# Kernel optimization log

Measured on AMD Instinct MI355X. Metric: run time of the kernel, lower is better.

Reference implementation:

```python
import jax, jax.numpy as jnp
import numpy as np

N = 100000
IN_DIM = 128
HID = 128
HEADS = 2
OUT_DIM = 2
E = 800000
NEG_SLOPE = 0.2


def setup_inputs() -> dict:
    key = jax.random.key(0)
    ks = jax.random.split(key, 12)
    x = jax.random.normal(ks[0], (N, IN_DIM), dtype=jnp.float32)
    edge_index = jax.random.randint(ks[1], (2, E), 0, N, dtype=jnp.int64)
    s = 0.05
    # GATConv layer 1: in=128 -> heads=2, out=128
    W1 = jax.random.normal(ks[2], (IN_DIM, HEADS * HID), dtype=jnp.float32) * s
    a_src1 = jax.random.normal(ks[3], (HEADS, HID), dtype=jnp.float32) * s
    a_dst1 = jax.random.normal(ks[4], (HEADS, HID), dtype=jnp.float32) * s
    b1 = jnp.zeros((HEADS * HID,), dtype=jnp.float32)
    # GATConv layer 2: in=256 -> heads=2, out=128
    W2 = jax.random.normal(ks[5], (HEADS * HID, HEADS * HID), dtype=jnp.float32) * s
    a_src2 = jax.random.normal(ks[6], (HEADS, HID), dtype=jnp.float32) * s
    a_dst2 = jax.random.normal(ks[7], (HEADS, HID), dtype=jnp.float32) * s
    b2 = jnp.zeros((HEADS * HID,), dtype=jnp.float32)
    # post_mp: Linear(256,128) -> Dropout(eval, no-op) -> Linear(128,2)
    Wp1 = jax.random.normal(ks[8], (HEADS * HID, HID), dtype=jnp.float32) * s
    bp1 = jnp.zeros((HID,), dtype=jnp.float32)
    Wp2 = jax.random.normal(ks[9], (HID, OUT_DIM), dtype=jnp.float32) * s
    bp2 = jnp.zeros((OUT_DIM,), dtype=jnp.float32)
    return {"x": x, "edge_index": edge_index,
            "W1": W1, "a_src1": a_src1, "a_dst1": a_dst1, "b1": b1,
            "W2": W2, "a_src2": a_src2, "a_dst2": a_dst2, "b2": b2,
            "Wp1": Wp1, "bp1": bp1, "Wp2": Wp2, "bp2": bp2}


def gat_conv(x, src, dst, W, a_src, a_dst, b):
    # linear transform, split heads: [N, H, C]
    h = (x @ W).reshape(-1, HEADS, HID)
    # per-node attention logits: [N, H]
    alpha_src = jnp.sum(h * a_src, axis=-1)
    alpha_dst = jnp.sum(h * a_dst, axis=-1)
    # per-edge logits, edge e = (src -> dst): [E, H]
    e = jax.nn.leaky_relu(alpha_src[src] + alpha_dst[dst], NEG_SLOPE)
    # segment softmax over incoming edges of each destination node
    m = jax.ops.segment_max(e, dst, num_segments=N)
    e = jnp.exp(e - m[dst])
    denom = jax.ops.segment_sum(e, dst, num_segments=N)
    alpha = e / (denom[dst] + 1e-16)
    # gather source features, weight, scatter-add to destinations
    msg = h[src] * alpha[:, :, None]            # [E, H, C]
    out = jax.ops.segment_sum(msg, dst, num_segments=N)  # [N, H, C]
    return out.reshape(-1, HEADS * HID) + b


def reference(x, edge_index, W1, a_src1, a_dst1, b1, W2, a_src2, a_dst2, b2,
              Wp1, bp1, Wp2, bp2):
    # add self-loops (PyG GATConv default)
    loops = jnp.arange(N, dtype=edge_index.dtype)
    src = jnp.concatenate([edge_index[0], loops])
    dst = jnp.concatenate([edge_index[1], loops])
    h = jax.nn.relu(gat_conv(x, src, dst, W1, a_src1, a_dst1, b1))
    h = jax.nn.relu(gat_conv(h, src, dst, W2, a_src2, a_dst2, b2))
    h = h @ Wp1 + bp1          # post_mp Linear 1 (dropout is eval no-op)
    h = h @ Wp2 + bp2          # post_mp Linear 2
    return jax.nn.sigmoid(h)
```

## Files before the change

### kernel.cpp

```cpp
#include <hip/hip_runtime.h>
#include <hip/hip_bf16.h>
#include <math.h>

#define NNODES 100000
#define NPAD   100032
#define IN_DIM 128
#define HID 128
#define HEADS 2
#define F2 256
#define NEDGES 800000
#define ETOT 900000
#define NEG_SLOPE 0.2f

typedef unsigned int uint;
typedef unsigned short ushort;
typedef __attribute__((ext_vector_type(8))) short short8;
typedef __attribute__((ext_vector_type(4))) float floatx4;

__device__ __forceinline__ ushort f2bf(float f) {
    uint u = __builtin_bit_cast(uint, f);
    u += 0x7fffu + ((u >> 16) & 1u);
    return (ushort)(u >> 16);
}
__device__ __forceinline__ float bf2f(uint u16) {
    return __builtin_bit_cast(float, u16 << 16);
}
__device__ __forceinline__ float wred_sum(float v) {
    for (int o = 32; o; o >>= 1) v += __shfl_xor(v, o);
    return v;
}

__global__ __launch_bounds__(256) void hist_kernel(const int* __restrict__ ei,
                                                   int* __restrict__ deg) {
    int i = blockIdx.x * 256 + threadIdx.x;
    if (i >= ETOT) return;
    int dst = (i < NEDGES) ? ei[NEDGES + i] : (i - NEDGES);
    atomicAdd(&deg[dst], 1);
}

__global__ __launch_bounds__(256) void scan1_kernel(const int* __restrict__ deg,
                                                    int* __restrict__ row_start,
                                                    int* __restrict__ bsum) {
    __shared__ int s[256];
    int t = threadIdx.x;
    int i = blockIdx.x * 256 + t;
    int v = (i < NNODES) ? deg[i] : 0;
    s[t] = v;
    __syncthreads();
    for (int off = 1; off < 256; off <<= 1) {
        int x = (t >= off) ? s[t - off] : 0;
        __syncthreads();
        s[t] += x;
        __syncthreads();
    }
    if (i < NNODES) row_start[i] = s[t] - v;
    if (t == 255) bsum[blockIdx.x] = s[255];
}

__global__ __launch_bounds__(256) void scan_fix_kernel(int* __restrict__ row_start,
                                                       const int* __restrict__ bsum,
                                                       int* __restrict__ cursor) {
    __shared__ int sh[256];
    int t = threadIdx.x, bid = blockIdx.x;
    int v = 0;
    for (int k = t; k < bid; k += 256) v += bsum[k];
    sh[t] = v;
    __syncthreads();
    for (int off = 128; off; off >>= 1) {
        if (t < off) sh[t] += sh[t + off];
        __syncthreads();
    }
    int boff = sh[0];
    int i = bid * 256 + t;
    if (i == 0) row_start[NNODES] = ETOT;
    if (i < NNODES) {
        int r = row_start[i] + boff;
        row_start[i] = r;
        cursor[i] = r;
    }
}

__global__ __launch_bounds__(256) void scatter_kernel(const int* __restrict__ ei,
                                                      int* __restrict__ cursor,
                                                      int* __restrict__ csr_src) {
    int i = blockIdx.x * 256 + threadIdx.x;
    if (i >= ETOT) return;
    int src, dst;
    if (i < NEDGES) { src = ei[i]; dst = ei[NEDGES + i]; }
    else            { src = i - NEDGES; dst = src; }
    int pos = atomicAdd(&cursor[dst], 1);
    csr_src[pos] = src;
}

__global__ __launch_bounds__(256) void prep_kernel(const float* __restrict__ W1,
                                                   ushort* __restrict__ W1t,
                                                   const float* __restrict__ W2,
                                                   ushort* __restrict__ W2t,
                                                   const float* __restrict__ Wp1,
                                                   const float* __restrict__ bp1,
                                                   const float* __restrict__ Wp2,
                                                   const float* __restrict__ bp2,
                                                   float2* __restrict__ Wf,
                                                   float* __restrict__ bfv,
                                                   int* __restrict__ deg) {
    int b = blockIdx.x, t = threadIdx.x;
    if (b < 128) {
        int i = b * 256 + t;
        int n = i >> 7, k = i & 127;
        W1t[n * 128 + k] = f2bf(W1[k * 256 + n]);
    } else if (b < 384) {
        int i = (b - 128) * 256 + t;
        int n = i >> 8, k = i & 255;
        W2t[n * 256 + k] = f2bf(W2[k * 256 + n]);
    } else if (b == 384) {
        float s0 = 0.f, s1 = 0.f;
        for (int m = 0; m < 128; m++) {
            float w = Wp1[t * 128 + m];
            s0 += w * Wp2[2 * m];
            s1 += w * Wp2[2 * m + 1];
        }
        Wf[t] = make_float2(s0, s1);
        if (t < 2) {
            float bb = bp2[t];
            for (int m = 0; m < 128; m++) bb += bp1[m] * Wp2[2 * m + t];
            bfv[t] = bb;
        }
    } else {
        int i = (b - 385) * 256 + t;
        if (i < NNODES) deg[i] = 0;
    }
}

__global__ __launch_bounds__(256) void mfma_gemm_f32A(const float* __restrict__ A,
                                                      const ushort* __restrict__ Bt,
                                                      ushort* __restrict__ C,
                                                      float* __restrict__ as_f,
                                                      float* __restrict__ ad_f,
                                                      const float* __restrict__ aS,
                                                      const float* __restrict__ aD,
                                                      int K) {
    __shared__ ushort As[64][40];
    __shared__ ushort Bs[128][40];
    int t = threadIdx.x;
    int wave = t >> 6, lane = t & 63;
    int quad = lane >> 4, l16 = lane & 15;
    size_t rowBase = (size_t)blockIdx.x * 64;
    int colBase = blockIdx.y * 128;
    int head = blockIdx.y;

    floatx4 acc[8];
#pragma unroll
    for (int i = 0; i < 8; i++) acc[i] = (floatx4){0.f, 0.f, 0.f, 0.f};

    int ar = t >> 2, ac = (t & 3) * 8;
    int agr = (int)rowBase + ar;
    const float*  Ap  = A + (size_t)agr * K + ac;
    const ushort* Bp0 = Bt + (size_t)(colBase + ar) * K + ac;
    const ushort* Bp1 = Bp0 + (size_t)64 * K;
    bool aok = agr < NNODES;

    for (int k0 = 0; k0 < K; k0 += 32) {
        float4 f0 = make_float4(0.f, 0.f, 0.f, 0.f), f1 = f0;
        if (aok) {
            f0 = *reinterpret_cast<const float4*>(Ap + k0);
            f1 = *reinterpret_cast<const float4*>(Ap + k0 + 4);
        }
        uint4 b0 = *reinterpret_cast<const uint4*>(Bp0 + k0);
        uint4 b1 = *reinterpret_cast<const uint4*>(Bp1 + k0);
        uint4 av;
        av.x = (uint)f2bf(f0.x) | ((uint)f2bf(f0.y) << 16);
        av.y = (uint)f2bf(f0.z) | ((uint)f2bf(f0.w) << 16);
        av.z = (uint)f2bf(f1.x) | ((uint)f2bf(f1.y) << 16);
        av.w = (uint)f2bf(f1.z) | ((uint)f2bf(f1.w) << 16);
        *reinterpret_cast<uint4*>(&As[ar][ac])      = av;
        *reinterpret_cast<uint4*>(&Bs[ar][ac])      = b0;
        *reinterpret_cast<uint4*>(&Bs[64 + ar][ac]) = b1;
        __syncthreads();

        union { uint4 u; short8 s; } afr, bfr;
        afr.u = *reinterpret_cast<const uint4*>(&As[wave * 16 + l16][quad * 8]);
#pragma unroll
        for (int nt = 0; nt < 8; nt++) {
            bfr.u = *reinterpret_cast<const uint4*>(&Bs[nt * 16 + l16][quad * 8]);
            acc[nt] = __builtin_amdgcn_mfma_f32_16x16x32_bf16(afr.s, bfr.s, acc[nt], 0, 0, 0);
        }
        __syncthreads();
    }

    {
        float aSv[8], aDv[8];
#pragma unroll
        for (int nt = 0; nt < 8; nt++) {
            int c = colBase + nt * 16 + l16;
            aSv[nt] = aS[c];
            aDv[nt] = aD[c];
        }
#pragma unroll
        for (int r = 0; r < 4; r++) {
            float ps = 0.f, pd = 0.f;
#pragma unroll
            for (int nt = 0; nt < 8; nt++) {
                ps += acc[nt][r] * aSv[nt];
                pd += acc[nt][r] * aDv[nt];
            }
#pragma unroll
            for (int o = 1; o < 16; o <<= 1) {
                ps += __shfl_xor(ps, o);
                pd += __shfl_xor(pd, o);
            }
            if (l16 == 0) {
                size_t row = rowBase + wave * 16 + quad * 4 + r;
                as_f[2 * row + head] = ps;
                ad_f[2 * row + head] = pd;
            }
        }
    }

    ushort* lbuf = &Bs[0][0];
#pragma unroll
    for (int half = 0; half < 2; half++) {
        __syncthreads();
#pragma unroll
        for (int nt4 = 0; nt4 < 4; nt4++) {
            int nt = half * 4 + nt4;
            int col = nt4 * 16 + l16;
#pragma unroll
            for (int r = 0; r < 4; r++) {
                int row = wave * 16 + quad * 4 + r;
                lbuf[row * 72 + col] = f2bf(acc[nt][r]);
            }
        }
        __syncthreads();
        int row = t >> 2;
        int ch = t & 3;
        uint4 v0 = *reinterpret_cast<const uint4*>(&lbuf[row * 72 + ch * 8]);
        uint4 v1 = *reinterpret_cast<const uint4*>(&lbuf[row * 72 + 32 + ch * 8]);
        size_t g = (rowBase + row) * (size_t)F2 + colBase + half * 64;
        *reinterpret_cast<uint4*>(&C[g + ch * 8]) = v0;
        *reinterpret_cast<uint4*>(&C[g + 32 + ch * 8]) = v1;
    }
}

__global__ __launch_bounds__(256) void mfma_gemm_bf16A(const ushort* __restrict__ A,
                                                       const ushort* __restrict__ Bt,
                                                       ushort* __restrict__ C,
                                                       float* __restrict__ as_f,
                                                       float* __restrict__ ad_f,
                                                       const float* __restrict__ aS,
                                                       const float* __restrict__ aD,
                                                       int K) {
    __shared__ ushort As[64][40];
    __shared__ ushort Bs[128][40];
    int t = threadIdx.x;
    int wave = t >> 6, lane = t & 63;
    int quad = lane >> 4, l16 = lane & 15;
    size_t rowBase = (size_t)blockIdx.x * 64;
    int colBase = blockIdx.y * 128;
    int head = blockIdx.y;

    floatx4 acc[8];
#pragma unroll
    for (int i = 0; i < 8; i++) acc[i] = (floatx4){0.f, 0.f, 0.f, 0.f};

    int ar = t >> 2, ac = (t & 3) * 8;
    const ushort* Ap  = A + (rowBase + ar) * K + ac;
    const ushort* Bp0 = Bt + (size_t)(colBase + ar) * K + ac;
    const ushort* Bp1 = Bp0 + (size_t)64 * K;

    for (int k0 = 0; k0 < K; k0 += 32) {
        uint4 av = *reinterpret_cast<const uint4*>(Ap + k0);
        uint4 b0 = *reinterpret_cast<const uint4*>(Bp0 + k0);
        uint4 b1 = *reinterpret_cast<const uint4*>(Bp1 + k0);
        *reinterpret_cast<uint4*>(&As[ar][ac])      = av;
        *reinterpret_cast<uint4*>(&Bs[ar][ac])      = b0;
        *reinterpret_cast<uint4*>(&Bs[64 + ar][ac]) = b1;
        __syncthreads();

        union { uint4 u; short8 s; } afr, bfr;
        afr.u = *reinterpret_cast<const uint4*>(&As[wave * 16 + l16][quad * 8]);
#pragma unroll
        for (int nt = 0; nt < 8; nt++) {
            bfr.u = *reinterpret_cast<const uint4*>(&Bs[nt * 16 + l16][quad * 8]);
            acc[nt] = __builtin_amdgcn_mfma_f32_16x16x32_bf16(afr.s, bfr.s, acc[nt], 0, 0, 0);
        }
        __syncthreads();
    }

    {
        float aSv[8], aDv[8];
#pragma unroll
        for (int nt = 0; nt < 8; nt++) {
            int c = colBase + nt * 16 + l16;
            aSv[nt] = aS[c];
            aDv[nt] = aD[c];
        }
#pragma unroll
        for (int r = 0; r < 4; r++) {
            float ps = 0.f, pd = 0.f;
#pragma unroll
            for (int nt = 0; nt < 8; nt++) {
                ps += acc[nt][r] * aSv[nt];
                pd += acc[nt][r] * aDv[nt];
            }
#pragma unroll
            for (int o = 1; o < 16; o <<= 1) {
                ps += __shfl_xor(ps, o);
                pd += __shfl_xor(pd, o);
            }
            if (l16 == 0) {
                size_t row = rowBase + wave * 16 + quad * 4 + r;
                as_f[2 * row + head] = ps;
                ad_f[2 * row + head] = pd;
            }
        }
    }

    ushort* lbuf = &Bs[0][0];
#pragma unroll
    for (int half = 0; half < 2; half++) {
        __syncthreads();
#pragma unroll
        for (int nt4 = 0; nt4 < 4; nt4++) {
            int nt = half * 4 + nt4;
            int col = nt4 * 16 + l16;
#pragma unroll
            for (int r = 0; r < 4; r++) {
                int row = wave * 16 + quad * 4 + r;
                lbuf[row * 72 + col] = f2bf(acc[nt][r]);
            }
        }
        __syncthreads();
        int row = t >> 2;
        int ch = t & 3;
        uint4 v0 = *reinterpret_cast<const uint4*>(&lbuf[row * 72 + ch * 8]);
        uint4 v1 = *reinterpret_cast<const uint4*>(&lbuf[row * 72 + 32 + ch * 8]);
        size_t g = (rowBase + row) * (size_t)F2 + colBase + half * 64;
        *reinterpret_cast<uint4*>(&C[g + ch * 8]) = v0;
        *reinterpret_cast<uint4*>(&C[g + 32 + ch * 8]) = v1;
    }
}

__device__ __forceinline__ float edge_w(float2 q, float adsel, bool head1) {
    float l = (head1 ? q.y : q.x) + adsel;
    l = l > 0.f ? l : NEG_SLOPE * l;
    return __expf(l);
}

__global__ __launch_bounds__(256) void gather_kernel(const uint2* __restrict__ hb2,
                                                     const int* __restrict__ row_start,
                                                     const int* __restrict__ csr_src,
                                                     const float2* __restrict__ as_,
                                                     const float2* __restrict__ ad_,
                                                     const float4* __restrict__ bias4,
                                                     uint2* __restrict__ outb2,
                                                     const float4* __restrict__ WfA,
                                                     const float* __restrict__ bfv,
                                                     float2* __restrict__ outp,
                                                     int final_mode) {
    int wave = threadIdx.x >> 6, lane = threadIdx.x & 63;
    int n = blockIdx.x * 4 + wave;
    if (n >= NNODES) return;
    int beg = row_start[n], end = row_start[n + 1];
    float2 ad = ad_[n];
    bool head1 = lane >= 32;
    float adsel = head1 ? ad.y : ad.x;

    float a0 = 0.f, a1 = 0.f, a2 = 0.f, a3 = 0.f;
    float aden = 0.f;

    int j = beg;
    for (; j + 3 < end; j += 4) {
        int s0 = csr_src[j],     s1 = csr_src[j + 1];
        int s2 = csr_src[j + 2], s3 = csr_src[j + 3];
        float2 q0 = as_[s0], q1 = as_[s1], q2 = as_[s2], q3 = as_[s3];
        uint2 h0 = hb2[(size_t)s0 * 64 + lane];
        uint2 h1 = hb2[(size_t)s1 * 64 + lane];
        uint2 h2 = hb2[(size_t)s2 * 64 + lane];
        uint2 h3 = hb2[(size_t)s3 * 64 + lane];
        float w0 = edge_w(q0, adsel, head1), w1 = edge_w(q1, adsel, head1);
        float w2 = edge_w(q2, adsel, head1), w3 = edge_w(q3, adsel, head1);
        aden += (w0 + w1) + (w2 + w3);
        a0 += w0 * bf2f(h0.x & 0xffffu) + w1 * bf2f(h1.x & 0xffffu)
            + w2 * bf2f(h2.x & 0xffffu) + w3 * bf2f(h3.x & 0xffffu);
        a1 += w0 * bf2f(h0.x >> 16) + w1 * bf2f(h1.x >> 16)
            + w2 * bf2f(h2.x >> 16) + w3 * bf2f(h3.x >> 16);
        a2 += w0 * bf2f(h0.y & 0xffffu) + w1 * bf2f(h1.y & 0xffffu)
            + w2 * bf2f(h2.y & 0xffffu) + w3 * bf2f(h3.y & 0xffffu);
        a3 += w0 * bf2f(h0.y >> 16) + w1 * bf2f(h1.y >> 16)
            + w2 * bf2f(h2.y >> 16) + w3 * bf2f(h3.y >> 16);
    }
    for (; j < end; j++) {
        int s = csr_src[j];
        float2 q = as_[s];
        uint2 hv = hb2[(size_t)s * 64 + lane];
        float w = edge_w(q, adsel, head1);
        aden += w;
        a0 += w * bf2f(hv.x & 0xffffu);
        a1 += w * bf2f(hv.x >> 16);
        a2 += w * bf2f(hv.y & 0xffffu);
        a3 += w * bf2f(hv.y >> 16);
    }

    float inv = 1.f / (aden + 1e-16f);
    float4 b = bias4[lane];
    float o0 = fmaxf(a0 * inv + b.x, 0.f);
    float o1 = fmaxf(a1 * inv + b.y, 0.f);
    float o2 = fmaxf(a2 * inv + b.z, 0.f);
    float o3 = fmaxf(a3 * inv + b.w, 0.f);
    if (!final_mode) {
        uint2 pk;
        pk.x = (uint)f2bf(o0) | ((uint)f2bf(o1) << 16);
        pk.y = (uint)f2bf(o2) | ((uint)f2bf(o3) << 16);
        outb2[(size_t)n * 64 + lane] = pk;
    } else {
        float4 wa = WfA[2 * lane];
        float4 wb = WfA[2 * lane + 1];
        float p0 = o0 * wa.x + o1 * wa.z + o2 * wb.x + o3 * wb.z;
        float p1 = o0 * wa.y + o1 * wa.w + o2 * wb.y + o3 * wb.w;
        p0 = wred_sum(p0);
        p1 = wred_sum(p1);
        if (lane == 0) {
            float2 r;
            r.x = 1.f / (1.f + __expf(-(p0 + bfv[0])));
            r.y = 1.f / (1.f + __expf(-(p1 + bfv[1])));
            outp[n] = r;
        }
    }
}

extern "C" void kernel_launch(void* const* d_in, const int* in_sizes, int n_in,
                              void* d_out, int out_size, void* d_ws, size_t ws_size,
                              hipStream_t stream) {
    const float* x      = (const float*)d_in[0];
    const int*   ei     = (const int*)d_in[1];
    const float* W1     = (const float*)d_in[2];
    const float* a_src1 = (const float*)d_in[3];
    const float* a_dst1 = (const float*)d_in[4];
    const float* b1     = (const float*)d_in[5];
    const float* W2     = (const float*)d_in[6];
    const float* a_src2 = (const float*)d_in[7];
    const float* a_dst2 = (const float*)d_in[8];
    const float* b2     = (const float*)d_in[9];
    const float* Wp1    = (const float*)d_in[10];
    const float* bp1    = (const float*)d_in[11];
    const float* Wp2    = (const float*)d_in[12];
    const float* bp2    = (const float*)d_in[13];
    float* outp = (float*)d_out;

    char* w = (char*)d_ws;
    ushort* hbf  = (ushort*)w; w += (size_t)NPAD * 256 * sizeof(ushort);
    ushort* obf  = (ushort*)w; w += (size_t)NPAD * 256 * sizeof(ushort);
    ushort* W1t  = (ushort*)w; w += (size_t)256 * 128 * sizeof(ushort);
    ushort* W2t  = (ushort*)w; w += (size_t)256 * 256 * sizeof(ushort);
    float2* Wf   = (float2*)w; w += 256 * sizeof(float2);
    float*  bfv  = (float*)w;  w += 4 * sizeof(float);
    float2* as_  = (float2*)w; w += (size_t)NPAD * sizeof(float2);
    float2* ad_  = (float2*)w; w += (size_t)NPAD * sizeof(float2);
    int* deg       = (int*)w; w += (size_t)NNODES * sizeof(int);
    int* row_start = (int*)w; w += (size_t)(NNODES + 16) * sizeof(int);
    int* cursor    = (int*)w; w += (size_t)NNODES * sizeof(int);
    int* csr_src   = (int*)w; w += (size_t)ETOT * sizeof(int);
    int* bsum      = (int*)w; w += 512 * sizeof(int);

    const int SCAN_BLOCKS = (NNODES + 255) / 256;
    const int NODE_WAVES  = (NNODES + 3) / 4;
    const int MB = NPAD / 64;

    prep_kernel<<<776, 256, 0, stream>>>(W1, W1t, W2, W2t, Wp1, bp1, Wp2, bp2,
                                         Wf, bfv, deg);

    hist_kernel<<<(ETOT + 255) / 256, 256, 0, stream>>>(ei, deg);
    scan1_kernel<<<SCAN_BLOCKS, 256, 0, stream>>>(deg, row_start, bsum);
    scan_fix_kernel<<<SCAN_BLOCKS, 256, 0, stream>>>(row_start, bsum, cursor);
    scatter_kernel<<<(ETOT + 255) / 256, 256, 0, stream>>>(ei, cursor, csr_src);

    mfma_gemm_f32A<<<dim3(MB, 2), 256, 0, stream>>>(x, W1t, hbf, (float*)as_, (float*)ad_,
                                                    a_src1, a_dst1, 128);
    gather_kernel<<<NODE_WAVES, 256, 0, stream>>>((const uint2*)hbf, row_start, csr_src,
                                                  as_, ad_, (const float4*)b1, (uint2*)obf,
                                                  (const float4*)Wf, bfv, (float2*)outp, 0);

    mfma_gemm_bf16A<<<dim3(MB, 2), 256, 0, stream>>>(obf, W2t, hbf, (float*)as_, (float*)ad_,
                                                     a_src2, a_dst2, 256);
    gather_kernel<<<NODE_WAVES, 256, 0, stream>>>((const uint2*)hbf, row_start, csr_src,
                                                  as_, ad_, (const float4*)b2, (uint2*)obf,
                                                  (const float4*)Wf, bfv, (float2*)outp, 1);
}
```

Baseline: 439.9 us.

## Double GEMM row tile to 128 so each wave computes two 16-row groups

Both MFMA GEMM kernels now process 128 rows per block instead of 64, and each wave keeps two sets of accumulators so every B fragment loaded from shared memory feeds two MFMAs. This halves B-tile global loads and LDS B reads per output, and halves the block count. NPAD grows to a multiple of 128 and the epilogue store is remapped to 128 rows. The cost is more accumulator registers, which may lower occupancy, and fewer blocks to spread over the CUs.

```diff
diff --git a/kernel.cpp b/kernel.cpp
--- a/kernel.cpp
+++ b/kernel.cpp
@@ -3,7 +3,7 @@
 #include <math.h>
 
 #define NNODES 100000
-#define NPAD   100032
+#define NPAD   100096
 #define IN_DIM 128
 #define HID 128
 #define HEADS 2
@@ -139,50 +139,64 @@
                                                       const float* __restrict__ aS,
                                                       const float* __restrict__ aD,
                                                       int K) {
-    __shared__ ushort As[64][40];
-    __shared__ ushort Bs[128][40];
+    __shared__ ushort smem[10240];
     int t = threadIdx.x;
     int wave = t >> 6, lane = t & 63;
     int quad = lane >> 4, l16 = lane & 15;
-    size_t rowBase = (size_t)blockIdx.x * 64;
+    size_t rowBase = (size_t)blockIdx.x * 128;
     int colBase = blockIdx.y * 128;
     int head = blockIdx.y;
 
-    floatx4 acc[8];
-#pragma unroll
-    for (int i = 0; i < 8; i++) acc[i] = (floatx4){0.f, 0.f, 0.f, 0.f};
+    floatx4 acc[2][8];
+#pragma unroll
+    for (int rg = 0; rg < 2; rg++)
+#pragma unroll
+        for (int i = 0; i < 8; i++) acc[rg][i] = (floatx4){0.f, 0.f, 0.f, 0.f};
 
     int ar = t >> 2, ac = (t & 3) * 8;
-    int agr = (int)rowBase + ar;
-    const float*  Ap  = A + (size_t)agr * K + ac;
+    int agr0 = (int)rowBase + ar;
+    const float*  Ap0 = A + (size_t)agr0 * K + ac;
+    const float*  Ap1 = Ap0 + (size_t)64 * K;
     const ushort* Bp0 = Bt + (size_t)(colBase + ar) * K + ac;
     const ushort* Bp1 = Bp0 + (size_t)64 * K;
-    bool aok = agr < NNODES;
+    bool aok0 = agr0 < NNODES;
+    bool aok1 = agr0 + 64 < NNODES;
 
     for (int k0 = 0; k0 < K; k0 += 32) {
-        float4 f0 = make_float4(0.f, 0.f, 0.f, 0.f), f1 = f0;
-        if (aok) {
-            f0 = *reinterpret_cast<const float4*>(Ap + k0);
-            f1 = *reinterpret_cast<const float4*>(Ap + k0 + 4);
+        float4 f0 = make_float4(0.f, 0.f, 0.f, 0.f), f1 = f0, f2 = f0, f3 = f0;
+        if (aok0) {
+            f0 = *reinterpret_cast<const float4*>(Ap0 + k0);
+            f1 = *reinterpret_cast<const float4*>(Ap0 + k0 + 4);
+        }
+        if (aok1) {
+            f2 = *reinterpret_cast<const float4*>(Ap1 + k0);
+            f3 = *reinterpret_cast<const float4*>(Ap1 + k0 + 4);
         }
         uint4 b0 = *reinterpret_cast<const uint4*>(Bp0 + k0);
         uint4 b1 = *reinterpret_cast<const uint4*>(Bp1 + k0);
-        uint4 av;
-        av.x = (uint)f2bf(f0.x) | ((uint)f2bf(f0.y) << 16);
-        av.y = (uint)f2bf(f0.z) | ((uint)f2bf(f0.w) << 16);
-        av.z = (uint)f2bf(f1.x) | ((uint)f2bf(f1.y) << 16);
-        av.w = (uint)f2bf(f1.z) | ((uint)f2bf(f1.w) << 16);
-        *reinterpret_cast<uint4*>(&As[ar][ac])      = av;
-        *reinterpret_cast<uint4*>(&Bs[ar][ac])      = b0;
-        *reinterpret_cast<uint4*>(&Bs[64 + ar][ac]) = b1;
-        __syncthreads();
-
-        union { uint4 u; short8 s; } afr, bfr;
-        afr.u = *reinterpret_cast<const uint4*>(&As[wave * 16 + l16][quad * 8]);
+        uint4 a0, a1;
+        a0.x = (uint)f2bf(f0.x) | ((uint)f2bf(f0.y) << 16);
+        a0.y = (uint)f2bf(f0.z) | ((uint)f2bf(f0.w) << 16);
+        a0.z = (uint)f2bf(f1.x) | ((uint)f2bf(f1.y) << 16);
+        a0.w = (uint)f2bf(f1.z) | ((uint)f2bf(f1.w) << 16);
+        a1.x = (uint)f2bf(f2.x) | ((uint)f2bf(f2.y) << 16);
+        a1.y = (uint)f2bf(f2.z) | ((uint)f2bf(f2.w) << 16);
+        a1.z = (uint)f2bf(f3.x) | ((uint)f2bf(f3.y) << 16);
+        a1.w = (uint)f2bf(f3.z) | ((uint)f2bf(f3.w) << 16);
+        *reinterpret_cast<uint4*>(&smem[ar * 40 + ac])          = a0;
+        *reinterpret_cast<uint4*>(&smem[(ar + 64) * 40 + ac])   = a1;
+        *reinterpret_cast<uint4*>(&smem[5120 + ar * 40 + ac])        = b0;
+        *reinterpret_cast<uint4*>(&smem[5120 + (ar + 64) * 40 + ac]) = b1;
+        __syncthreads();
+
+        union { uint4 u; short8 s; } afr0, afr1, bfr;
+        afr0.u = *reinterpret_cast<const uint4*>(&smem[(wave * 32 + l16) * 40 + quad * 8]);
+        afr1.u = *reinterpret_cast<const uint4*>(&smem[(wave * 32 + 16 + l16) * 40 + quad * 8]);
 #pragma unroll
         for (int nt = 0; nt < 8; nt++) {
-            bfr.u = *reinterpret_cast<const uint4*>(&Bs[nt * 16 + l16][quad * 8]);
-            acc[nt] = __builtin_amdgcn_mfma_f32_16x16x32_bf16(afr.s, bfr.s, acc[nt], 0, 0, 0);
+            bfr.u = *reinterpret_cast<const uint4*>(&smem[5120 + (nt * 16 + l16) * 40 + quad * 8]);
+            acc[0][nt] = __builtin_amdgcn_mfma_f32_16x16x32_bf16(afr0.s, bfr.s, acc[0][nt], 0, 0, 0);
+            acc[1][nt] = __builtin_amdgcn_mfma_f32_16x16x32_bf16(afr1.s, bfr.s, acc[1][nt], 0, 0, 0);
         }
         __syncthreads();
     }
@@ -196,27 +210,29 @@
             aDv[nt] = aD[c];
         }
 #pragma unroll
-        for (int r = 0; r < 4; r++) {
-            float ps = 0.f, pd = 0.f;
-#pragma unroll
-            for (int nt = 0; nt < 8; nt++) {
-                ps += acc[nt][r] * aSv[nt];
-                pd += acc[nt][r] * aDv[nt];
+        for (int rg = 0; rg < 2; rg++) {
+#pragma unroll
+            for (int r = 0; r < 4; r++) {
+                float ps = 0.f, pd = 0.f;
+#pragma unroll
+                for (int nt = 0; nt < 8; nt++) {
+                    ps += acc[rg][nt][r] * aSv[nt];
+                    pd += acc[rg][nt][r] * aDv[nt];
+                }
+#pragma unroll
+                for (int o = 1; o < 16; o <<= 1) {
+                    ps += __shfl_xor(ps, o);
+                    pd += __shfl_xor(pd, o);
+                }
+                if (l16 == 0) {
+                    size_t row = rowBase + wave * 32 + rg * 16 + quad * 4 + r;
+                    as_f[2 * row + head] = ps;
+                    ad_f[2 * row + head] = pd;
+                }
             }
-#pragma unroll
-            for (int o = 1; o < 16; o <<= 1) {
-                ps += __shfl_xor(ps, o);
-                pd += __shfl_xor(pd, o);
-            }
-            if (l16 == 0) {
-                size_t row = rowBase + wave * 16 + quad * 4 + r;
-                as_f[2 * row + head] = ps;
-                ad_f[2 * row + head] = pd;
-            }
-        }
-    }
-
-    ushort* lbuf = &Bs[0][0];
+        }
+    }
+
 #pragma unroll
     for (int half = 0; half < 2; half++) {
         __syncthreads();
@@ -225,19 +241,21 @@
             int nt = half * 4 + nt4;
             int col = nt4 * 16 + l16;
 #pragma unroll
-            for (int r = 0; r < 4; r++) {
-                int row = wave * 16 + quad * 4 + r;
-                lbuf[row * 72 + col] = f2bf(acc[nt][r]);
+            for (int rg = 0; rg < 2; rg++) {
+#pragma unroll
+                for (int r = 0; r < 4; r++) {
+                    int row = wave * 32 + rg * 16 + quad * 4 + r;
+                    smem[row * 72 + col] = f2bf(acc[rg][nt][r]);
+                }
             }
         }
         __syncthreads();
-        int row = t >> 2;
-        int ch = t & 3;
-        uint4 v0 = *reinterpret_cast<const uint4*>(&lbuf[row * 72 + ch * 8]);
-        uint4 v1 = *reinterpret_cast<const uint4*>(&lbuf[row * 72 + 32 + ch * 8]);
-        size_t g = (rowBase + row) * (size_t)F2 + colBase + half * 64;
-        *reinterpret_cast<uint4*>(&C[g + ch * 8]) = v0;
-        *reinterpret_cast<uint4*>(&C[g + 32 + ch * 8]) = v1;
+        int row = t >> 1;
+        int ch = (t & 1) * 4;
+        const uint4* src = reinterpret_cast<const uint4*>(&smem[row * 72]);
+        uint4 v0 = src[ch], v1 = src[ch + 1], v2 = src[ch + 2], v3 = src[ch + 3];
+        uint4* dst = reinterpret_cast<uint4*>(&C[(rowBase + row) * (size_t)F2 + colBase + half * 64]);
+        dst[ch] = v0; dst[ch + 1] = v1; dst[ch + 2] = v2; dst[ch + 3] = v3;
     }
 }
 
@@ -249,39 +267,45 @@
                                                        const float* __restrict__ aS,
                                                        const float* __restrict__ aD,
                                                        int K) {
-    __shared__ ushort As[64][40];
-    __shared__ ushort Bs[128][40];
+    __shared__ ushort smem[10240];
     int t = threadIdx.x;
     int wave = t >> 6, lane = t & 63;
     int quad = lane >> 4, l16 = lane & 15;
-    size_t rowBase = (size_t)blockIdx.x * 64;
+    size_t rowBase = (size_t)blockIdx.x * 128;
     int colBase = blockIdx.y * 128;
     int head = blockIdx.y;
 
-    floatx4 acc[8];
-#pragma unroll
-    for (int i = 0; i < 8; i++) acc[i] = (floatx4){0.f, 0.f, 0.f, 0.f};
+    floatx4 acc[2][8];
+#pragma unroll
+    for (int rg = 0; rg < 2; rg++)
+#pragma unroll
+        for (int i = 0; i < 8; i++) acc[rg][i] = (floatx4){0.f, 0.f, 0.f, 0.f};
 
     int ar = t >> 2, ac = (t & 3) * 8;
-    const ushort* Ap  = A + (rowBase + ar) * K + ac;
+    const ushort* Ap0 = A + (rowBase + ar) * K + ac;
+    const ushort* Ap1 = Ap0 + (size_t)64 * K;
     const ushort* Bp0 = Bt + (size_t)(colBase + ar) * K + ac;
     const ushort* Bp1 = Bp0 + (size_t)64 * K;
 
     for (int k0 = 0; k0 < K; k0 += 32) {
-        uint4 av = *reinterpret_cast<const uint4*>(Ap + k0);
+        uint4 a0 = *reinterpret_cast<const uint4*>(Ap0 + k0);
+        uint4 a1 = *reinterpret_cast<const uint4*>(Ap1 + k0);
         uint4 b0 = *reinterpret_cast<const uint4*>(Bp0 + k0);
         uint4 b1 = *reinterpret_cast<const uint4*>(Bp1 + k0);
-        *reinterpret_cast<uint4*>(&As[ar][ac])      = av;
-        *reinterpret_cast<uint4*>(&Bs[ar][ac])      = b0;
-        *reinterpret_cast<uint4*>(&Bs[64 + ar][ac]) = b1;
-        __syncthreads();
-
-        union { uint4 u; short8 s; } afr, bfr;
-        afr.u = *reinterpret_cast<const uint4*>(&As[wave * 16 + l16][quad * 8]);
+        *reinterpret_cast<uint4*>(&smem[ar * 40 + ac])          = a0;
+        *reinterpret_cast<uint4*>(&smem[(ar + 64) * 40 + ac])   = a1;
+        *reinterpret_cast<uint4*>(&smem[5120 + ar * 40 + ac])        = b0;
+        *reinterpret_cast<uint4*>(&smem[5120 + (ar + 64) * 40 + ac]) = b1;
+        __syncthreads();
+
+        union { uint4 u; short8 s; } afr0, afr1, bfr;
+        afr0.u = *reinterpret_cast<const uint4*>(&smem[(wave * 32 + l16) * 40 + quad * 8]);
+        afr1.u = *reinterpret_cast<const uint4*>(&smem[(wave * 32 + 16 + l16) * 40 + quad * 8]);
 #pragma unroll
         for (int nt = 0; nt < 8; nt++) {
-            bfr.u = *reinterpret_cast<const uint4*>(&Bs[nt * 16 + l16][quad * 8]);
-            acc[nt] = __builtin_amdgcn_mfma_f32_16x16x32_bf16(afr.s, bfr.s, acc[nt], 0, 0, 0);
+            bfr.u = *reinterpret_cast<const uint4*>(&smem[5120 + (nt * 16 + l16) * 40 + quad * 8]);
+            acc[0][nt] = __builtin_amdgcn_mfma_f32_16x16x32_bf16(afr0.s, bfr.s, acc[0][nt], 0, 0, 0);
+            acc[1][nt] = __builtin_amdgcn_mfma_f32_16x16x32_bf16(afr1.s, bfr.s, acc[1][nt], 0, 0, 0);
         }
         __syncthreads();
     }
@@ -295,27 +319,29 @@
             aDv[nt] = aD[c];
         }
 #pragma unroll
-        for (int r = 0; r < 4; r++) {
-            float ps = 0.f, pd = 0.f;
-#pragma unroll
-            for (int nt = 0; nt < 8; nt++) {
-                ps += acc[nt][r] * aSv[nt];
-                pd += acc[nt][r] * aDv[nt];
+        for (int rg = 0; rg < 2; rg++) {
+#pragma unroll
+            for (int r = 0; r < 4; r++) {
+                float ps = 0.f, pd = 0.f;
+#pragma unroll
+                for (int nt = 0; nt < 8; nt++) {
+                    ps += acc[rg][nt][r] * aSv[nt];
+                    pd += acc[rg][nt][r] * aDv[nt];
+                }
+#pragma unroll
+                for (int o = 1; o < 16; o <<= 1) {
+                    ps += __shfl_xor(ps, o);
+                    pd += __shfl_xor(pd, o);
+                }
+                if (l16 == 0) {
+                    size_t row = rowBase + wave * 32 + rg * 16 + quad * 4 + r;
+                    as_f[2 * row + head] = ps;
+                    ad_f[2 * row + head] = pd;
+                }
             }
-#pragma unroll
-            for (int o = 1; o < 16; o <<= 1) {
-                ps += __shfl_xor(ps, o);
-                pd += __shfl_xor(pd, o);
-            }
-            if (l16 == 0) {
-                size_t row = rowBase + wave * 16 + quad * 4 + r;
-                as_f[2 * row + head] = ps;
-                ad_f[2 * row + head] = pd;
-            }
-        }
-    }
-
-    ushort* lbuf = &Bs[0][0];
+        }
+    }
+
 #pragma unroll
     for (int half = 0; half < 2; half++) {
         __syncthreads();
@@ -324,19 +350,21 @@
             int nt = half * 4 + nt4;
             int col = nt4 * 16 + l16;
 #pragma unroll
-            for (int r = 0; r < 4; r++) {
-                int row = wave * 16 + quad * 4 + r;
-                lbuf[row * 72 + col] = f2bf(acc[nt][r]);
+            for (int rg = 0; rg < 2; rg++) {
+#pragma unroll
+                for (int r = 0; r < 4; r++) {
+                    int row = wave * 32 + rg * 16 + quad * 4 + r;
+                    smem[row * 72 + col] = f2bf(acc[rg][nt][r]);
+                }
             }
         }
         __syncthreads();
-        int row = t >> 2;
-        int ch = t & 3;
-        uint4 v0 = *reinterpret_cast<const uint4*>(&lbuf[row * 72 + ch * 8]);
-        uint4 v1 = *reinterpret_cast<const uint4*>(&lbuf[row * 72 + 32 + ch * 8]);
-        size_t g = (rowBase + row) * (size_t)F2 + colBase + half * 64;
-        *reinterpret_cast<uint4*>(&C[g + ch * 8]) = v0;
-        *reinterpret_cast<uint4*>(&C[g + 32 + ch * 8]) = v1;
+        int row = t >> 1;
+        int ch = (t & 1) * 4;
+        const uint4* src = reinterpret_cast<const uint4*>(&smem[row * 72]);
+        uint4 v0 = src[ch], v1 = src[ch + 1], v2 = src[ch + 2], v3 = src[ch + 3];
+        uint4* dst = reinterpret_cast<uint4*>(&C[(rowBase + row) * (size_t)F2 + colBase + half * 64]);
+        dst[ch] = v0; dst[ch + 1] = v1; dst[ch + 2] = v2; dst[ch + 3] = v3;
     }
 }
 
@@ -464,7 +492,7 @@
 
     const int SCAN_BLOCKS = (NNODES + 255) / 256;
     const int NODE_WAVES  = (NNODES + 3) / 4;
-    const int MB = NPAD / 64;
+    const int MB = NPAD / 128;
 
     prep_kernel<<<776, 256, 0, stream>>>(W1, W1t, W2, W2t, Wp1, bp1, Wp2, bp2,
                                          Wf, bfv, deg);
```

New measurement: 453.7 us. 3.1% more time.

## Pre-convert x to bf16, use direct global-to-LDS loads in unified GEMM, split gathers

Applied to the files above, without the earlier changes.

Adds a conversion pass in the prep kernel that writes x as bf16 into a new workspace buffer, so both GEMMs share one kernel taking bf16 A. That kernel now fills LDS with global_load_lds 16-byte transfers into an XOR-swizzled unpadded layout instead of staging through registers. Each gather launch is split into two half-range launches. The aim is to drop register staging and the per-tile fp32-to-bf16 conversion; the cost is an extra full pass over x, additional launches, and the xbf rows beyond NNODES in the padded buffer are never written.

```diff
diff --git a/kernel.cpp b/kernel.cpp
--- a/kernel.cpp
+++ b/kernel.cpp
@@ -28,6 +28,13 @@
 __device__ __forceinline__ float wred_sum(float v) {
     for (int o = 32; o; o >>= 1) v += __shfl_xor(v, o);
     return v;
+}
+
+__device__ __forceinline__ void gld16(const ushort* g, ushort* l) {
+    __builtin_amdgcn_global_load_lds(
+        (const __attribute__((address_space(1))) unsigned int*)(uintptr_t)g,
+        (__attribute__((address_space(3))) unsigned int*)(unsigned int)(uintptr_t)l,
+        16, 0, 0);
 }
 
 __global__ __launch_bounds__(256) void hist_kernel(const int* __restrict__ ei,
@@ -102,6 +109,8 @@
                                                    const float* __restrict__ bp2,
                                                    float2* __restrict__ Wf,
                                                    float* __restrict__ bfv,
+                                                   const float* __restrict__ x,
+                                                   ushort* __restrict__ xbf,
                                                    int* __restrict__ deg) {
     int b = blockIdx.x, t = threadIdx.x;
     if (b < 128) {
@@ -125,22 +134,31 @@
             for (int m = 0; m < 128; m++) bb += bp1[m] * Wp2[2 * m + t];
             bfv[t] = bb;
         }
+    } else if (b < 6635) {
+        size_t i = (size_t)(b - 385) * 2048 + t * 8;
+        float4 f0 = *reinterpret_cast<const float4*>(&x[i]);
+        float4 f1 = *reinterpret_cast<const float4*>(&x[i + 4]);
+        uint4 o;
+        o.x = (uint)f2bf(f0.x) | ((uint)f2bf(f0.y) << 16);
+        o.y = (uint)f2bf(f0.z) | ((uint)f2bf(f0.w) << 16);
+        o.z = (uint)f2bf(f1.x) | ((uint)f2bf(f1.y) << 16);
+        o.w = (uint)f2bf(f1.z) | ((uint)f2bf(f1.w) << 16);
+        *reinterpret_cast<uint4*>(&xbf[i]) = o;
     } else {
-        int i = (b - 385) * 256 + t;
+        int i = (b - 6635) * 256 + t;
         if (i < NNODES) deg[i] = 0;
     }
 }
 
-__global__ __launch_bounds__(256) void mfma_gemm_f32A(const float* __restrict__ A,
-                                                      const ushort* __restrict__ Bt,
-                                                      ushort* __restrict__ C,
-                                                      float* __restrict__ as_f,
-                                                      float* __restrict__ ad_f,
-                                                      const float* __restrict__ aS,
-                                                      const float* __restrict__ aD,
-                                                      int K) {
-    __shared__ ushort As[64][40];
-    __shared__ ushort Bs[128][40];
+__global__ __launch_bounds__(256) void mfma_gemm(const ushort* __restrict__ A,
+                                                 const ushort* __restrict__ Bt,
+                                                 ushort* __restrict__ C,
+                                                 float* __restrict__ as_f,
+                                                 float* __restrict__ ad_f,
+                                                 const float* __restrict__ aS,
+                                                 const float* __restrict__ aD,
+                                                 int K) {
+    __shared__ ushort smem[6144];
     int t = threadIdx.x;
     int wave = t >> 6, lane = t & 63;
     int quad = lane >> 4, l16 = lane & 15;
@@ -152,36 +170,30 @@
 #pragma unroll
     for (int i = 0; i < 8; i++) acc[i] = (floatx4){0.f, 0.f, 0.f, 0.f};
 
-    int ar = t >> 2, ac = (t & 3) * 8;
-    int agr = (int)rowBase + ar;
-    const float*  Ap  = A + (size_t)agr * K + ac;
-    const ushort* Bp0 = Bt + (size_t)(colBase + ar) * K + ac;
-    const ushort* Bp1 = Bp0 + (size_t)64 * K;
-    bool aok = agr < NNODES;
+    int srow = lane >> 2;
+    int scg  = (lane & 3) ^ ((lane >> 3) & 3);
+    const ushort* gA  = A  + (rowBase + wave * 16 + srow) * (size_t)K + scg * 8;
+    const ushort* gB0 = Bt + (size_t)(colBase + wave * 16 + srow) * K + scg * 8;
+    const ushort* gB1 = gB0 + (size_t)64 * K;
+    ushort* lA  = smem + wave * 512;
+    ushort* lB0 = smem + 2048 + wave * 512;
+    ushort* lB1 = lB0 + 2048;
+
+    const char* sb = (const char*)smem;
+    int xs = (quad ^ ((l16 >> 1) & 3)) * 16;
+    int aoff = (wave * 16 + l16) * 64 + xs;
+    int boff = 4096 + l16 * 64 + xs;
 
     for (int k0 = 0; k0 < K; k0 += 32) {
-        float4 f0 = make_float4(0.f, 0.f, 0.f, 0.f), f1 = f0;
-        if (aok) {
-            f0 = *reinterpret_cast<const float4*>(Ap + k0);
-            f1 = *reinterpret_cast<const float4*>(Ap + k0 + 4);
-        }
-        uint4 b0 = *reinterpret_cast<const uint4*>(Bp0 + k0);
-        uint4 b1 = *reinterpret_cast<const uint4*>(Bp1 + k0);
-        uint4 av;
-        av.x = (uint)f2bf(f0.x) | ((uint)f2bf(f0.y) << 16);
-        av.y = (uint)f2bf(f0.z) | ((uint)f2bf(f0.w) << 16);
-        av.z = (uint)f2bf(f1.x) | ((uint)f2bf(f1.y) << 16);
-        av.w = (uint)f2bf(f1.z) | ((uint)f2bf(f1.w) << 16);
-        *reinterpret_cast<uint4*>(&As[ar][ac])      = av;
-        *reinterpret_cast<uint4*>(&Bs[ar][ac])      = b0;
-        *reinterpret_cast<uint4*>(&Bs[64 + ar][ac]) = b1;
-        __syncthreads();
-
+        gld16(gA + k0, lA);
+        gld16(gB0 + k0, lB0);
+        gld16(gB1 + k0, lB1);
+        __syncthreads();
         union { uint4 u; short8 s; } afr, bfr;
-        afr.u = *reinterpret_cast<const uint4*>(&As[wave * 16 + l16][quad * 8]);
+        afr.u = *reinterpret_cast<const uint4*>(sb + aoff);
 #pragma unroll
         for (int nt = 0; nt < 8; nt++) {
-            bfr.u = *reinterpret_cast<const uint4*>(&Bs[nt * 16 + l16][quad * 8]);
+            bfr.u = *reinterpret_cast<const uint4*>(sb + boff + nt * 1024);
             acc[nt] = __builtin_amdgcn_mfma_f32_16x16x32_bf16(afr.s, bfr.s, acc[nt], 0, 0, 0);
         }
         __syncthreads();
@@ -216,106 +228,7 @@
         }
     }
 
-    ushort* lbuf = &Bs[0][0];
-#pragma unroll
-    for (int half = 0; half < 2; half++) {
-        __syncthreads();
-#pragma unroll
-        for (int nt4 = 0; nt4 < 4; nt4++) {
-            int nt = half * 4 + nt4;
-            int col = nt4 * 16 + l16;
-#pragma unroll
-            for (int r = 0; r < 4; r++) {
-                int row = wave * 16 + quad * 4 + r;
-                lbuf[row * 72 + col] = f2bf(acc[nt][r]);
-            }
-        }
-        __syncthreads();
-        int row = t >> 2;
-        int ch = t & 3;
-        uint4 v0 = *reinterpret_cast<const uint4*>(&lbuf[row * 72 + ch * 8]);
-        uint4 v1 = *reinterpret_cast<const uint4*>(&lbuf[row * 72 + 32 + ch * 8]);
-        size_t g = (rowBase + row) * (size_t)F2 + colBase + half * 64;
-        *reinterpret_cast<uint4*>(&C[g + ch * 8]) = v0;
-        *reinterpret_cast<uint4*>(&C[g + 32 + ch * 8]) = v1;
-    }
-}
-
-__global__ __launch_bounds__(256) void mfma_gemm_bf16A(const ushort* __restrict__ A,
-                                                       const ushort* __restrict__ Bt,
-                                                       ushort* __restrict__ C,
-                                                       float* __restrict__ as_f,
-                                                       float* __restrict__ ad_f,
-                                                       const float* __restrict__ aS,
-                                                       const float* __restrict__ aD,
-                                                       int K) {
-    __shared__ ushort As[64][40];
-    __shared__ ushort Bs[128][40];
-    int t = threadIdx.x;
-    int wave = t >> 6, lane = t & 63;
-    int quad = lane >> 4, l16 = lane & 15;
-    size_t rowBase = (size_t)blockIdx.x * 64;
-    int colBase = blockIdx.y * 128;
-    int head = blockIdx.y;
-
-    floatx4 acc[8];
-#pragma unroll
-    for (int i = 0; i < 8; i++) acc[i] = (floatx4){0.f, 0.f, 0.f, 0.f};
-
-    int ar = t >> 2, ac = (t & 3) * 8;
-    const ushort* Ap  = A + (rowBase + ar) * K + ac;
-    const ushort* Bp0 = Bt + (size_t)(colBase + ar) * K + ac;
-    const ushort* Bp1 = Bp0 + (size_t)64 * K;
-
-    for (int k0 = 0; k0 < K; k0 += 32) {
-        uint4 av = *reinterpret_cast<const uint4*>(Ap + k0);
-        uint4 b0 = *reinterpret_cast<const uint4*>(Bp0 + k0);
-        uint4 b1 = *reinterpret_cast<const uint4*>(Bp1 + k0);
-        *reinterpret_cast<uint4*>(&As[ar][ac])      = av;
-        *reinterpret_cast<uint4*>(&Bs[ar][ac])      = b0;
-        *reinterpret_cast<uint4*>(&Bs[64 + ar][ac]) = b1;
-        __syncthreads();
-
-        union { uint4 u; short8 s; } afr, bfr;
-        afr.u = *reinterpret_cast<const uint4*>(&As[wave * 16 + l16][quad * 8]);
-#pragma unroll
-        for (int nt = 0; nt < 8; nt++) {
-            bfr.u = *reinterpret_cast<const uint4*>(&Bs[nt * 16 + l16][quad * 8]);
-            acc[nt] = __builtin_amdgcn_mfma_f32_16x16x32_bf16(afr.s, bfr.s, acc[nt], 0, 0, 0);
-        }
-        __syncthreads();
-    }
-
-    {
-        float aSv[8], aDv[8];
-#pragma unroll
-        for (int nt = 0; nt < 8; nt++) {
-            int c = colBase + nt * 16 + l16;
-            aSv[nt] = aS[c];
-            aDv[nt] = aD[c];
-        }
-#pragma unroll
-        for (int r = 0; r < 4; r++) {
-            float ps = 0.f, pd = 0.f;
-#pragma unroll
-            for (int nt = 0; nt < 8; nt++) {
-                ps += acc[nt][r] * aSv[nt];
-                pd += acc[nt][r] * aDv[nt];
-            }
-#pragma unroll
-            for (int o = 1; o < 16; o <<= 1) {
-                ps += __shfl_xor(ps, o);
-                pd += __shfl_xor(pd, o);
-            }
-            if (l16 == 0) {
-                size_t row = rowBase + wave * 16 + quad * 4 + r;
-                as_f[2 * row + head] = ps;
-                ad_f[2 * row + head] = pd;
-            }
-        }
-    }
-
-    ushort* lbuf = &Bs[0][0];
+    ushort* lbuf = smem;
 #pragma unroll
     for (int half = 0; half < 2; half++) {
         __syncthreads();
@@ -356,10 +269,11 @@
                                                      const float4* __restrict__ WfA,
                                                      const float* __restrict__ bfv,
                                                      float2* __restrict__ outp,
-                                                     int final_mode) {
+                                                     int final_mode,
+                                                     int nbase, int nlimit) {
     int wave = threadIdx.x >> 6, lane = threadIdx.x & 63;
-    int n = blockIdx.x * 4 + wave;
-    if (n >= NNODES) return;
+    int n = nbase + blockIdx.x * 4 + wave;
+    if (n >= nlimit) return;
     int beg = row_start[n], end = row_start[n + 1];
     float2 ad = ad_[n];
     bool head1 = lane >= 32;
@@ -448,6 +362,7 @@
     float* outp = (float*)d_out;
 
     char* w = (char*)d_ws;
+    ushort* xbf  = (ushort*)w; w += (size_t)NPAD * 128 * sizeof(ushort);
     ushort* hbf  = (ushort*)w; w += (size_t)NPAD * 256 * sizeof(ushort);
     ushort* obf  = (ushort*)w; w += (size_t)NPAD * 256 * sizeof(ushort);
     ushort* W1t  = (ushort*)w; w += (size_t)256 * 128 * sizeof(ushort);
@@ -463,26 +378,36 @@
     int* bsum      = (int*)w; w += 512 * sizeof(int);
 
     const int SCAN_BLOCKS = (NNODES + 255) / 256;
-    const int NODE_WAVES  = (NNODES + 3) / 4;
+    const int HALF_BLOCKS = 12500;
     const int MB = NPAD / 64;
 
-    prep_kernel<<<776, 256, 0, stream>>>(W1, W1t, W2, W2t, Wp1, bp1, Wp2, bp2,
-                                         Wf, bfv, deg);
+    prep_kernel<<<7026, 256, 0, stream>>>(W1, W1t, W2, W2t, Wp1, bp1, Wp2, bp2,
+                                          Wf, bfv, x, xbf, deg);
 
     hist_kernel<<<(ETOT + 255) / 256, 256, 0, stream>>>(ei, deg);
     scan1_kernel<<<SCAN_BLOCKS, 256, 0, stream>>>(deg, row_start, bsum);
     scan_fix_kernel<<<SCAN_BLOCKS, 256, 0, stream>>>(row_start, bsum, cursor);
     scatter_kernel<<<(ETOT + 255) / 256, 256, 0, stream>>>(ei, cursor, csr_src);
 
-    mfma_gemm_f32A<<<dim3(MB, 2), 256, 0, stream>>>(x, W1t, hbf, (float*)as_, (float*)ad_,
-                                                    a_src1, a_dst1, 128);
-    gather_kernel<<<NODE_WAVES, 256, 0, stream>>>((const uint2*)hbf, row_start, csr_src,
-                                                  as_, ad_, (const float4*)b1, (uint2*)obf,
-                                                  (const float4*)Wf, bfv, (float2*)outp, 0);
-
-    mfma_gemm_bf16A<<<dim3(MB, 2), 256, 0, stream>>>(obf, W2t, hbf, (float*)as_, (float*)ad_,
-                                                     a_src2, a_dst2, 256);
-    gather_kernel<<<NODE_WAVES, 256, 0, stream>>>((const uint2*)hbf, row_start, csr_src,
-                                                  as_, ad_, (const float4*)b2, (uint2*)obf,
-                                                  (const float4*)Wf, bfv, (float2*)outp, 1);
-}
+    mfma_gemm<<<dim3(MB, 2), 256, 0, stream>>>(xbf, W1t, hbf, (float*)as_, (float*)ad_,
+                                               a_src1, a_dst1, 128);
+    gather_kernel<<<HALF_BLOCKS, 256, 0, stream>>>((const uint2*)hbf, row_start, csr_src,
+                                                   as_, ad_, (const float4*)b1, (uint2*)obf,
+                                                   (const float4*)Wf, bfv, (float2*)outp,
+                                                   0, 0, 50000);
+    gather_kernel<<<HALF_BLOCKS, 256, 0, stream>>>((const uint2*)hbf, row_start, csr_src,
+                                                   as_, ad_, (const float4*)b1, (uint2*)obf,
+                                                   (const float4*)Wf, bfv, (float2*)outp,
+                                                   0, 50000, NNODES);
+
+    mfma_gemm<<<dim3(MB, 2), 256, 0, stream>>>(obf, W2t, hbf, (float*)as_, (float*)ad_,
+                                               a_src2, a_dst2, 256);
+    gather_kernel<<<HALF_BLOCKS, 256, 0, stream>>>((const uint2*)hbf, row_start, csr_src,
+                                                   as_, ad_, (const float4*)b2, (uint2*)obf,
+                                                   (const float4*)Wf, bfv, (float2*)outp,
+                                                   1, 0, 50000);
+    gather_kernel<<<HALF_BLOCKS, 256, 0, stream>>>((const uint2*)hbf, row_start, csr_src,
+                                                   as_, ad_, (const float4*)b2, (uint2*)obf,
+                                                   (const float4*)Wf, bfv, (float2*)outp,
+                                                   1, 50000, NNODES);
+}
```

Result: no change. 448.2 us (+1.9%).
